# Kernel tuning notes

Measured on AMD Instinct MI355X. Metric: run time of the kernel, lower is better.

Reference implementation:

```python
import jax, jax.numpy as jnp
import numpy as np

B, S, D = 2, 2048, 1024
H, E = 16, 64


def setup_inputs() -> dict:
    key = jax.random.key(0)
    k1, k2, k3, k4 = jax.random.split(key, 4)
    x = jax.random.normal(k1, (B, S, D), dtype=jnp.float32)
    # per-head Q/K/V projection weights, stacked over the head axis
    scale = 1.0 / np.sqrt(D)
    Wq = jax.random.normal(k2, (H, D, E), dtype=jnp.float32) * scale
    Wk = jax.random.normal(k3, (H, D, E), dtype=jnp.float32) * scale
    Wv = jax.random.normal(k4, (H, D, E), dtype=jnp.float32) * scale
    return {"x": x, "Wq": Wq, "Wk": Wk, "Wv": Wv}


def reference(x, Wq, Wk, Wv):
    # Grouped-over-heads equivalent of the per-head torch loop.
    q = jnp.einsum("bsd,hde->bhse", x, Wq)  # [B,H,S,E]
    k = jnp.einsum("bsd,hde->bhse", x, Wk)
    v = jnp.einsum("bsd,hde->bhse", x, Wv)

    scores = jnp.einsum("bhse,bhte->bhst", q, k)  # [B,H,S,S]
    scores = scores / jnp.sqrt(jnp.asarray(E, dtype=scores.dtype))
    causal = jnp.tril(jnp.ones((S, S), dtype=bool))  # True on/below diagonal
    scores = jnp.where(causal, scores, jnp.finfo(scores.dtype).min)
    attn = jax.nn.softmax(scores, axis=-1)  # dropout p=0.0 -> identity

    out = jnp.einsum("bhst,bhte->bhse", attn, v)  # [B,H,S,E]
    # concat over heads on the last dim, matching torch.concat(..., dim=-1)
    return out.transpose(0, 2, 1, 3).reshape(B, S, H * E)
```

## Files before the change

### kernel.cpp

```cpp
#include <hip/hip_runtime.h>
#include <stdint.h>

#define S_LEN 2048
#define D_DIM 1024
#define NB 2
#define NH 16
#define NE 64
#define N_COLS (3 * NH * NE)
#define K_DIM D_DIM

typedef unsigned short u16;
typedef unsigned int u32;
typedef u16 u16x8 __attribute__((ext_vector_type(8)));
typedef __bf16 bf16x8 __attribute__((ext_vector_type(8)));
typedef __bf16 bf16x4 __attribute__((ext_vector_type(4)));
typedef float f32x4 __attribute__((ext_vector_type(4)));

__device__ __forceinline__ u16 f2b(float f) {
  u32 u = __builtin_bit_cast(u32, f);
  return (u16)((u + 0x7FFFu + ((u >> 16) & 1u)) >> 16);
}

__device__ __forceinline__ void gload_lds16(const void* g, void* l) {
  __builtin_amdgcn_global_load_lds(
      (const __attribute__((address_space(1))) u32*)g,
      (__attribute__((address_space(3))) u32*)l, 16, 0, 0);
}

__global__ __launch_bounds__(256) void k_prep(const float* __restrict__ x,
                                              const float* __restrict__ Wq,
                                              const float* __restrict__ Wk,
                                              const float* __restrict__ Wv,
                                              u16* __restrict__ xb,
                                              u16* __restrict__ Wt) {
  __shared__ u16 tile[64][65];
  int bid = blockIdx.x;
  int t = threadIdx.x;
  if (bid < 2048) {
    size_t i = (size_t)bid * 256 + t;
    const float4* xf = (const float4*)x;
    float4 a = xf[2 * i], c = xf[2 * i + 1];
    u16x8 o;
    o[0] = f2b(a.x); o[1] = f2b(a.y); o[2] = f2b(a.z); o[3] = f2b(a.w);
    o[4] = f2b(c.x); o[5] = f2b(c.y); o[6] = f2b(c.z); o[7] = f2b(c.w);
    *(u16x8*)(xb + 8 * i) = o;
  } else {
    int wbid = bid - 2048;
    int kb = wbid & 15;
    int h = (wbid >> 4) & 15;
    int proj = wbid >> 8;
    const float* W = (proj == 0) ? Wq : ((proj == 1) ? Wk : Wv);
    int k0 = kb * 64;
    int e = t & 63, kr = t >> 6;
    const float* src = W + ((size_t)h * D_DIM + k0 + kr * 16) * NE + e;
#pragma unroll
    for (int j = 0; j < 16; ++j) tile[kr * 16 + j][e] = f2b(src[(size_t)j * NE]);
    __syncthreads();
    int e2 = t >> 2, kc = (t & 3) * 16;
    u16x8 o0, o1;
#pragma unroll
    for (int j = 0; j < 8; ++j) { o0[j] = tile[kc + j][e2]; o1[j] = tile[kc + 8 + j][e2]; }
    size_t n = (size_t)proj * 1024 + h * 64 + e2;
    u16* dst = Wt + n * K_DIM + k0 + kc;
    *(u16x8*)dst = o0;
    *(u16x8*)(dst + 8) = o1;
  }
}

__global__ __launch_bounds__(256) void k_gemm(const u16* __restrict__ A,
                                              const u16* __restrict__ Bt,
                                              u16* __restrict__ C) {
  __shared__ __align__(16) u16 As[128 * 64];
  __shared__ __align__(16) u16 Bs[128 * 64];
  int t = threadIdx.x;
  int lane = t & 63, w = t >> 6;
  int wr = (w >> 1) * 64, wc = (w & 1) * 64;
  int bid = blockIdx.x;
  int xcd = bid & 7, r0 = bid >> 3;
  int m0 = (r0 / 3) * 128;
  int n0 = (xcd * 3 + (r0 % 3)) * 128;
  float qscale = ((n0 + wc) < 1024) ? 0.18033688f : 1.0f;
  f32x4 acc[4][4];
#pragma unroll
  for (int m = 0; m < 4; m++)
#pragma unroll
    for (int n = 0; n < 4; n++)
#pragma unroll
      for (int j = 0; j < 4; j++) acc[m][n][j] = 0.f;

  for (int k0 = 0; k0 < K_DIM; k0 += 64) {
#pragma unroll
    for (int i = 0; i < 4; ++i) {
      int ci = i * 256 + t;
      int row = ci >> 3, c = ci & 7;
      int cs = c ^ (row & 7);
      gload_lds16(A + (size_t)(m0 + row) * K_DIM + k0 + cs * 8,
                  (char*)As + (size_t)(i * 256 + w * 64) * 16);
      gload_lds16(Bt + (size_t)(n0 + row) * K_DIM + k0 + cs * 8,
                  (char*)Bs + (size_t)(i * 256 + w * 64) * 16);
    }
    __syncthreads();
#pragma unroll
    for (int ks = 0; ks < 2; ++ks) {
      int kc = ks * 4 + (lane >> 4);
      bf16x8 af[4], bfr[4];
#pragma unroll
      for (int m = 0; m < 4; m++) {
        int r = wr + m * 16 + (lane & 15);
        af[m] = *(const bf16x8*)&As[r * 64 + ((kc ^ (r & 7)) * 8)];
      }
#pragma unroll
      for (int n = 0; n < 4; n++) {
        int r = wc + n * 16 + (lane & 15);
        bfr[n] = *(const bf16x8*)&Bs[r * 64 + ((kc ^ (r & 7)) * 8)];
      }
#pragma unroll
      for (int m = 0; m < 4; m++)
#pragma unroll
        for (int n = 0; n < 4; n++)
          acc[m][n] = __builtin_amdgcn_mfma_f32_16x16x32_bf16(af[m], bfr[n], acc[m][n], 0, 0, 0);
    }
    __syncthreads();
  }
#pragma unroll
  for (int m = 0; m < 4; m++) {
#pragma unroll
    for (int r = 0; r < 4; r++) {
      int row = m0 + wr + m * 16 + (lane >> 4) * 4 + r;
#pragma unroll
      for (int n = 0; n < 4; n++) {
        int col = n0 + wc + n * 16 + (lane & 15);
        C[(size_t)row * N_COLS + col] = f2b(acc[m][n][r] * qscale);
      }
    }
  }
}

__device__ __forceinline__ void stage_k(const u16* kb_, u16* kdst, int kv0, int t, int w) {
#pragma unroll
  for (int i = 0; i < 2; ++i) {
    int ci = i * 256 + t;
    int row = ci >> 3, c = ci & 7;
    int cs = c ^ (row & 7);
    gload_lds16(kb_ + (size_t)(kv0 + row) * N_COLS + cs * 8,
                (char*)kdst + (size_t)(i * 256 + w * 64) * 16);
  }
}

__device__ __forceinline__ void vwrite(u16* vt, u16x8 va, u16x8 vb2, int vp, int vec) {
#pragma unroll
  for (int j = 0; j < 8; ++j) {
    int e = vec * 8 + j;
    int slot = (vp >> 2) ^ (e & 7) ^ (e >> 3);
    *(u32*)((char*)vt + e * 128 + slot * 16 + (vp & 3) * 4) =
        (u32)va[j] | ((u32)vb2[j] << 16);
  }
}

__global__ __launch_bounds__(256) void k_attn(const u16* __restrict__ qkv,
                                              float* __restrict__ out) {
  __shared__ __align__(16) u16 Ks[2][64 * 64];
  __shared__ __align__(16) u16 Vt[2][64 * 64];
  int t = threadIdx.x;
  int lane = t & 63, w = t >> 6;
  int hi = lane >> 4, l15 = lane & 15;
  int bid = blockIdx.x;
  int x = bid & 7, g = bid >> 3;
  int bh = x * 4 + (g & 3);
  int qt = 31 - (g >> 2);
  int b = bh >> 4, h = bh & 15;
  const u16* qb_ = qkv + (size_t)b * S_LEN * N_COLS + h * NE;
  const u16* kb_ = qb_ + 1024;
  const u16* vb_ = qb_ + 2048;
  int vp = t >> 3, vec = t & 7;

  int q0 = qt * 64;
  int nt = qt + 1;
  int wqb = q0 + w * 16;

  bf16x8 qf[2];
#pragma unroll
  for (int ks = 0; ks < 2; ks++)
    qf[ks] = *(const bf16x8*)(qb_ + (size_t)(wqb + l15) * N_COLS + ks * 32 + hi * 8);

  f32x4 o[4];
#pragma unroll
  for (int i = 0; i < 4; i++)
#pragma unroll
    for (int j = 0; j < 4; j++) o[i][j] = 0.f;
  float lsum = 0.f;
  int myq = wqb + l15;

  stage_k(kb_, Ks[0], 0, t, w);
  {
    const u16* vs = vb_ + (size_t)(2 * vp) * N_COLS + vec * 8;
    u16x8 va = *(const u16x8*)vs;
    u16x8 vb2 = *(const u16x8*)(vs + N_COLS);
    vwrite(Vt[0], va, vb2, vp, vec);
  }
  __syncthreads();

  int cur = 0;
  for (int ti = 0; ti < nt; ++ti) {
    int kv0 = ti * 64;
    bool pf = (ti + 1 < nt);
    u16x8 va, vb2;
    if (pf) {
      const u16* vs = vb_ + (size_t)(kv0 + 64 + 2 * vp) * N_COLS + vec * 8;
      va = *(const u16x8*)vs;
      vb2 = *(const u16x8*)(vs + N_COLS);
      stage_k(kb_, Ks[cur ^ 1], kv0 + 64, t, w);
    }

    f32x4 s[4];
#pragma unroll
    for (int f = 0; f < 4; f++)
#pragma unroll
      for (int j = 0; j < 4; j++) s[f][j] = 0.f;
    __builtin_amdgcn_s_setprio(1);
#pragma unroll
    for (int ks = 0; ks < 2; ks++) {
      int kc = ks * 4 + hi;
#pragma unroll
      for (int f = 0; f < 4; f++) {
        int r = f * 16 + l15;
        bf16x8 kf = *(const bf16x8*)&Ks[cur][r * 64 + ((kc ^ (r & 7)) * 8)];
        s[f] = __builtin_amdgcn_mfma_f32_16x16x32_bf16(kf, qf[ks], s[f], 0, 0, 0);
      }
    }
    __builtin_amdgcn_s_setprio(0);

    bool diag = (ti == nt - 1);
#pragma unroll
    for (int f = 0; f < 4; f++) {
#pragma unroll
      for (int r = 0; r < 4; r++) {
        float p = __builtin_amdgcn_exp2f(s[f][r]);
        if (diag) {
          int kv = kv0 + f * 16 + 4 * hi + r;
          p = (kv <= myq) ? p : 0.f;
        }
        s[f][r] = p;
        lsum += p;
      }
    }

    if (pf) vwrite(Vt[cur ^ 1], va, vb2, vp, vec);

    __builtin_amdgcn_s_setprio(1);
#pragma unroll
    for (int ks = 0; ks < 2; ks++) {
      bf16x8 pa;
#pragma unroll
      for (int j = 0; j < 4; j++) {
        pa[j] = (__bf16)s[2 * ks][j];
        pa[4 + j] = (__bf16)s[2 * ks + 1][j];
      }
      int kvo1 = 32 * ks + 4 * hi;
      int kvo2 = kvo1 + 16;
#pragma unroll
      for (int ef = 0; ef < 4; ef++) {
        int e = ef * 16 + l15;
        int sw = (e & 7) ^ (e >> 3);
        int a1 = e * 128 + (((kvo1 >> 3) ^ sw) * 16) + (kvo1 & 7) * 2;
        int a2 = e * 128 + (((kvo2 >> 3) ^ sw) * 16) + (kvo2 & 7) * 2;
        bf16x4 vlo = *(const bf16x4*)((const char*)Vt[cur] + a1);
        bf16x4 vhi = *(const bf16x4*)((const char*)Vt[cur] + a2);
        bf16x8 vbf;
#pragma unroll
        for (int j = 0; j < 4; j++) { vbf[j] = vlo[j]; vbf[4 + j] = vhi[j]; }
        o[ef] = __builtin_amdgcn_mfma_f32_16x16x32_bf16(pa, vbf, o[ef], 0, 0, 0);
      }
    }
    __builtin_amdgcn_s_setprio(0);
    __syncthreads();
    cur ^= 1;
  }

  lsum += __shfl_xor(lsum, 16);
  lsum += __shfl_xor(lsum, 32);
#pragma unroll
  for (int r = 0; r < 4; r++) {
    float l = __shfl(lsum, 4 * hi + r);
    float inv = 1.0f / l;
    int q = wqb + 4 * hi + r;
#pragma unroll
    for (int ef = 0; ef < 4; ef++) {
      int col = h * NE + ef * 16 + l15;
      out[((size_t)b * S_LEN + q) * (NH * NE) + col] = o[ef][r] * inv;
    }
  }
}

extern "C" void kernel_launch(void* const* d_in, const int* in_sizes, int n_in,
                              void* d_out, int out_size, void* d_ws, size_t ws_size,
                              hipStream_t stream) {
  const float* x = (const float*)d_in[0];
  const float* Wq = (const float*)d_in[1];
  const float* Wk = (const float*)d_in[2];
  const float* Wv = (const float*)d_in[3];
  float* out = (float*)d_out;

  char* ws = (char*)d_ws;
  u16* xb = (u16*)ws;
  u16* Wt = (u16*)(ws + (8u << 20));
  u16* qkv = (u16*)(ws + (14u << 20));

  k_prep<<<dim3(2816), dim3(256), 0, stream>>>(x, Wq, Wk, Wv, xb, Wt);
  k_gemm<<<dim3(768), dim3(256), 0, stream>>>(xb, Wt, qkv);
  k_attn<<<dim3(1024), dim3(256), 0, stream>>>(qkv, out);
}
```

Measured before the change: 93.92 us.

## Split KV range of long causal query tiles across two blocks with a fixup kernel

Measured after the change: 100.2 us. +6.7%, slower.

```diff
diff --git a/kernel.cpp b/kernel.cpp
--- a/kernel.cpp
+++ b/kernel.cpp
@@ -158,16 +158,27 @@
 }
 
 __global__ __launch_bounds__(256) void k_attn(const u16* __restrict__ qkv,
-                                              float* __restrict__ out) {
+                                              float* __restrict__ out,
+                                              float* __restrict__ O0,
+                                              float* __restrict__ l0,
+                                              float* __restrict__ l1) {
   __shared__ __align__(16) u16 Ks[2][64 * 64];
   __shared__ __align__(16) u16 Vt[2][64 * 64];
   int t = threadIdx.x;
   int lane = t & 63, w = t >> 6;
   int hi = lane >> 4, l15 = lane & 15;
   int bid = blockIdx.x;
-  int x = bid & 7, g = bid >> 3;
-  int bh = x * 4 + (g & 3);
-  int qt = 31 - (g >> 2);
+  int x = bid & 7, r_ = bid >> 3;
+  int bh = x * 4 + (r_ & 3);
+  int u = r_ >> 2;
+  int qt, c;
+  if (u < 32) { qt = 31 - (u >> 1); c = u & 1; }
+  else        { qt = 47 - u;        c = 0;     }
+  int nt = qt + 1;
+  int halfn = (nt + 1) >> 1;
+  bool split = (u < 32);
+  int lo = (split && c) ? halfn : 0;
+  int te = split ? (c ? nt : halfn) : nt;
   int b = bh >> 4, h = bh & 15;
   const u16* qb_ = qkv + (size_t)b * S_LEN * N_COLS + h * NE;
   const u16* kb_ = qb_ + 1024;
@@ -175,7 +186,6 @@
   int vp = t >> 3, vec = t & 7;
 
   int q0 = qt * 64;
-  int nt = qt + 1;
   int wqb = q0 + w * 16;
 
   bf16x8 qf[2];
@@ -191,9 +201,9 @@
   float lsum = 0.f;
   int myq = wqb + l15;
 
-  stage_k(kb_, Ks[0], 0, t, w);
+  stage_k(kb_, Ks[0], lo * 64, t, w);
   {
-    const u16* vs = vb_ + (size_t)(2 * vp) * N_COLS + vec * 8;
+    const u16* vs = vb_ + (size_t)(lo * 64 + 2 * vp) * N_COLS + vec * 8;
     u16x8 va = *(const u16x8*)vs;
     u16x8 vb2 = *(const u16x8*)(vs + N_COLS);
     vwrite(Vt[0], va, vb2, vp, vec);
@@ -201,9 +211,9 @@
   __syncthreads();
 
   int cur = 0;
-  for (int ti = 0; ti < nt; ++ti) {
+  for (int ti = lo; ti < te; ++ti) {
     int kv0 = ti * 64;
-    bool pf = (ti + 1 < nt);
+    bool pf = (ti + 1 < te);
     u16x8 va, vb2;
     if (pf) {
       const u16* vs = vb_ + (size_t)(kv0 + 64 + 2 * vp) * N_COLS + vec * 8;
@@ -279,17 +289,66 @@
 
   lsum += __shfl_xor(lsum, 16);
   lsum += __shfl_xor(lsum, 32);
-#pragma unroll
-  for (int r = 0; r < 4; r++) {
-    float l = __shfl(lsum, 4 * hi + r);
-    float inv = 1.0f / l;
-    int q = wqb + 4 * hi + r;
-#pragma unroll
-    for (int ef = 0; ef < 4; ef++) {
-      int col = h * NE + ef * 16 + l15;
-      out[((size_t)b * S_LEN + q) * (NH * NE) + col] = o[ef][r] * inv;
-    }
-  }
+
+  if (!split) {
+#pragma unroll
+    for (int r = 0; r < 4; r++) {
+      float l = __shfl(lsum, 4 * hi + r);
+      float inv = 1.0f / l;
+      int q = wqb + 4 * hi + r;
+#pragma unroll
+      for (int ef = 0; ef < 4; ef++) {
+        int col = h * NE + ef * 16 + l15;
+        out[((size_t)b * S_LEN + q) * (NH * NE) + col] = o[ef][r] * inv;
+      }
+    }
+  } else {
+    int sp = bh * 16 + (qt - 16);
+    if (c == 0) {
+#pragma unroll
+      for (int r = 0; r < 4; r++) {
+        int row = w * 16 + 4 * hi + r;
+#pragma unroll
+        for (int ef = 0; ef < 4; ef++)
+          O0[(size_t)sp * 4096 + row * 64 + ef * 16 + l15] = o[ef][r];
+      }
+      if (lane < 16) l0[sp * 64 + w * 16 + l15] = lsum;
+    } else {
+#pragma unroll
+      for (int r = 0; r < 4; r++) {
+        int q = wqb + 4 * hi + r;
+#pragma unroll
+        for (int ef = 0; ef < 4; ef++) {
+          int col = h * NE + ef * 16 + l15;
+          out[((size_t)b * S_LEN + q) * (NH * NE) + col] = o[ef][r];
+        }
+      }
+      if (lane < 16) l1[sp * 64 + w * 16 + l15] = lsum;
+    }
+  }
+}
+
+__global__ __launch_bounds__(256) void k_fix(float* __restrict__ out,
+                                             const float* __restrict__ O0,
+                                             const float* __restrict__ l0,
+                                             const float* __restrict__ l1) {
+  int f = (blockIdx.x * 256 + threadIdx.x) * 4;
+  int sp = f >> 12;
+  int row = (f >> 6) & 63;
+  int e0 = f & 63;
+  int bh = sp >> 4, qt = 16 + (sp & 15);
+  int b = bh >> 4, h = bh & 15;
+  int q = qt * 64 + row;
+  float inv = 1.0f / (l0[sp * 64 + row] + l1[sp * 64 + row]);
+  float4 p0 = *(const float4*)&O0[(size_t)sp * 4096 + row * 64 + e0];
+  size_t oi = ((size_t)b * S_LEN + q) * (NH * NE) + h * NE + e0;
+  float4 cu = *(float4*)&out[oi];
+  float4 res;
+  res.x = (cu.x + p0.x) * inv;
+  res.y = (cu.y + p0.y) * inv;
+  res.z = (cu.z + p0.z) * inv;
+  res.w = (cu.w + p0.w) * inv;
+  *(float4*)&out[oi] = res;
 }
 
 extern "C" void kernel_launch(void* const* d_in, const int* in_sizes, int n_in,
@@ -305,8 +364,12 @@
   u16* xb = (u16*)ws;
   u16* Wt = (u16*)(ws + (8u << 20));
   u16* qkv = (u16*)(ws + (14u << 20));
+  float* O0 = (float*)ws;
+  float* l0 = (float*)(ws + (8u << 20));
+  float* l1 = (float*)(ws + (8u << 20) + (128u << 10));
 
   k_prep<<<dim3(2816), dim3(256), 0, stream>>>(x, Wq, Wk, Wv, xb, Wt);
   k_gemm<<<dim3(768), dim3(256), 0, stream>>>(xb, Wt, qkv);
-  k_attn<<<dim3(1024), dim3(256), 0, stream>>>(qkv, out);
-}
+  k_attn<<<dim3(1536), dim3(256), 0, stream>>>(qkv, out, O0, l0, l1);
+  k_fix<<<dim3(2048), dim3(256), 0, stream>>>(out, O0, l0, l1);
+}
```

## Process two 64-row query tiles per attention block to reuse K/V tiles

Applied to the files above, without the earlier changes.

Result: slower. 132.1 us (+40.7%).

```diff
diff --git a/kernel.cpp b/kernel.cpp
--- a/kernel.cpp
+++ b/kernel.cpp
@@ -13,7 +13,6 @@
 typedef unsigned int u32;
 typedef u16 u16x8 __attribute__((ext_vector_type(8)));
 typedef __bf16 bf16x8 __attribute__((ext_vector_type(8)));
-typedef __bf16 bf16x4 __attribute__((ext_vector_type(4)));
 typedef float f32x4 __attribute__((ext_vector_type(4)));
 
 __device__ __forceinline__ u16 f2b(float f) {
@@ -147,12 +146,14 @@
   }
 }
 
-__device__ __forceinline__ void vwrite(u16* vt, u16x8 va, u16x8 vb2, int vp, int vec) {
+__device__ __forceinline__ void vwrite(u16* vt, u16x8 va, u16x8 vb2, int kvA, int vec) {
+  int pi_hi = ((kvA >> 5) << 2) | ((kvA & 15) >> 2);
+  int pi_lo = (kvA & 3) * 4;
 #pragma unroll
   for (int j = 0; j < 8; ++j) {
     int e = vec * 8 + j;
-    int slot = (vp >> 2) ^ (e & 7) ^ (e >> 3);
-    *(u32*)((char*)vt + e * 128 + slot * 16 + (vp & 3) * 4) =
+    int sw = (e & 7) ^ (e >> 3);
+    *(u32*)((char*)vt + e * 128 + ((pi_hi ^ sw) * 16) + pi_lo) =
         (u32)va[j] | ((u32)vb2[j] << 16);
   }
 }
@@ -167,36 +168,39 @@
   int bid = blockIdx.x;
   int x = bid & 7, g = bid >> 3;
   int bh = x * 4 + (g & 3);
-  int qt = 31 - (g >> 2);
+  int qb = 15 - (g >> 2);
   int b = bh >> 4, h = bh & 15;
   const u16* qb_ = qkv + (size_t)b * S_LEN * N_COLS + h * NE;
   const u16* kb_ = qb_ + 1024;
   const u16* vb_ = qb_ + 2048;
-  int vp = t >> 3, vec = t & 7;
-
-  int q0 = qt * 64;
-  int nt = qt + 1;
-  int wqb = q0 + w * 16;
-
-  bf16x8 qf[2];
-#pragma unroll
-  for (int ks = 0; ks < 2; ks++)
-    qf[ks] = *(const bf16x8*)(qb_ + (size_t)(wqb + l15) * N_COLS + ks * 32 + hi * 8);
-
-  f32x4 o[4];
+  int w2 = t >> 3, vec = t & 7;
+  int kvA0 = (w2 & 15) | ((w2 & 16) << 1);
+
+  int q0 = qb * 128;
+  int nt = 2 * qb + 2;
+  int wqA = q0 + w * 16;
+  int myqA = wqA + l15, myqB = myqA + 64;
+
+  bf16x8 qfA[2], qfB[2];
+#pragma unroll
+  for (int ks = 0; ks < 2; ks++) {
+    qfA[ks] = *(const bf16x8*)(qb_ + (size_t)(wqA + l15) * N_COLS + ks * 32 + hi * 8);
+    qfB[ks] = *(const bf16x8*)(qb_ + (size_t)(wqA + 64 + l15) * N_COLS + ks * 32 + hi * 8);
+  }
+
+  f32x4 oA[4], oB[4];
 #pragma unroll
   for (int i = 0; i < 4; i++)
 #pragma unroll
-    for (int j = 0; j < 4; j++) o[i][j] = 0.f;
-  float lsum = 0.f;
-  int myq = wqb + l15;
+    for (int j = 0; j < 4; j++) { oA[i][j] = 0.f; oB[i][j] = 0.f; }
+  float lsA = 0.f, lsB = 0.f;
 
   stage_k(kb_, Ks[0], 0, t, w);
   {
-    const u16* vs = vb_ + (size_t)(2 * vp) * N_COLS + vec * 8;
+    const u16* vs = vb_ + (size_t)kvA0 * N_COLS + vec * 8;
     u16x8 va = *(const u16x8*)vs;
-    u16x8 vb2 = *(const u16x8*)(vs + N_COLS);
-    vwrite(Vt[0], va, vb2, vp, vec);
+    u16x8 vb2 = *(const u16x8*)(vs + 16 * N_COLS);
+    vwrite(Vt[0], va, vb2, kvA0, vec);
   }
   __syncthreads();
 
@@ -206,17 +210,20 @@
     bool pf = (ti + 1 < nt);
     u16x8 va, vb2;
     if (pf) {
-      const u16* vs = vb_ + (size_t)(kv0 + 64 + 2 * vp) * N_COLS + vec * 8;
+      const u16* vs = vb_ + (size_t)(kv0 + 64 + kvA0) * N_COLS + vec * 8;
       va = *(const u16x8*)vs;
-      vb2 = *(const u16x8*)(vs + N_COLS);
+      vb2 = *(const u16x8*)(vs + 16 * N_COLS);
       stage_k(kb_, Ks[cur ^ 1], kv0 + 64, t, w);
     }
-
-    f32x4 s[4];
+    bool doA = (ti != nt - 1);
+    bool maskA = (ti == nt - 2);
+    bool maskB = (ti == nt - 1);
+
+    f32x4 sA[4], sB[4];
 #pragma unroll
     for (int f = 0; f < 4; f++)
 #pragma unroll
-      for (int j = 0; j < 4; j++) s[f][j] = 0.f;
+      for (int j = 0; j < 4; j++) { sA[f][j] = 0.f; sB[f][j] = 0.f; }
     __builtin_amdgcn_s_setprio(1);
 #pragma unroll
     for (int ks = 0; ks < 2; ks++) {
@@ -225,51 +232,60 @@
       for (int f = 0; f < 4; f++) {
         int r = f * 16 + l15;
         bf16x8 kf = *(const bf16x8*)&Ks[cur][r * 64 + ((kc ^ (r & 7)) * 8)];
-        s[f] = __builtin_amdgcn_mfma_f32_16x16x32_bf16(kf, qf[ks], s[f], 0, 0, 0);
+        sB[f] = __builtin_amdgcn_mfma_f32_16x16x32_bf16(kf, qfB[ks], sB[f], 0, 0, 0);
+        if (doA)
+          sA[f] = __builtin_amdgcn_mfma_f32_16x16x32_bf16(kf, qfA[ks], sA[f], 0, 0, 0);
       }
     }
     __builtin_amdgcn_s_setprio(0);
 
-    bool diag = (ti == nt - 1);
-#pragma unroll
-    for (int f = 0; f < 4; f++) {
+    if (doA) {
+#pragma unroll
+      for (int f = 0; f < 4; f++)
+#pragma unroll
+        for (int r = 0; r < 4; r++) {
+          float p = __builtin_amdgcn_exp2f(sA[f][r]);
+          if (maskA) {
+            int kv = kv0 + f * 16 + 4 * hi + r;
+            p = (kv <= myqA) ? p : 0.f;
+          }
+          sA[f][r] = p;
+          lsA += p;
+        }
+    }
+#pragma unroll
+    for (int f = 0; f < 4; f++)
 #pragma unroll
       for (int r = 0; r < 4; r++) {
-        float p = __builtin_amdgcn_exp2f(s[f][r]);
-        if (diag) {
+        float p = __builtin_amdgcn_exp2f(sB[f][r]);
+        if (maskB) {
           int kv = kv0 + f * 16 + 4 * hi + r;
-          p = (kv <= myq) ? p : 0.f;
+          p = (kv <= myqB) ? p : 0.f;
         }
-        s[f][r] = p;
-        lsum += p;
-      }
-    }
-
-    if (pf) vwrite(Vt[cur ^ 1], va, vb2, vp, vec);
+        sB[f][r] = p;
+        lsB += p;
+      }
+
+    if (pf) vwrite(Vt[cur ^ 1], va, vb2, kvA0, vec);
 
     __builtin_amdgcn_s_setprio(1);
 #pragma unroll
     for (int ks = 0; ks < 2; ks++) {
-      bf16x8 pa;
-#pragma unroll
-      for (int j = 0; j < 4; j++) {
-        pa[j] = (__bf16)s[2 * ks][j];
-        pa[4 + j] = (__bf16)s[2 * ks + 1][j];
-      }
-      int kvo1 = 32 * ks + 4 * hi;
-      int kvo2 = kvo1 + 16;
+      bf16x8 paA, paB;
+#pragma unroll
+      for (int d = 0; d < 8; d++) {
+        paA[d] = (__bf16)sA[2 * ks + (d & 1)][d >> 1];
+        paB[d] = (__bf16)sB[2 * ks + (d & 1)][d >> 1];
+      }
 #pragma unroll
       for (int ef = 0; ef < 4; ef++) {
         int e = ef * 16 + l15;
         int sw = (e & 7) ^ (e >> 3);
-        int a1 = e * 128 + (((kvo1 >> 3) ^ sw) * 16) + (kvo1 & 7) * 2;
-        int a2 = e * 128 + (((kvo2 >> 3) ^ sw) * 16) + (kvo2 & 7) * 2;
-        bf16x4 vlo = *(const bf16x4*)((const char*)Vt[cur] + a1);
-        bf16x4 vhi = *(const bf16x4*)((const char*)Vt[cur] + a2);
-        bf16x8 vbf;
-#pragma unroll
-        for (int j = 0; j < 4; j++) { vbf[j] = vlo[j]; vbf[4 + j] = vhi[j]; }
-        o[ef] = __builtin_amdgcn_mfma_f32_16x16x32_bf16(pa, vbf, o[ef], 0, 0, 0);
+        bf16x8 vbf = *(const bf16x8*)((const char*)Vt[cur] + e * 128 +
+                                      (((4 * ks + hi) ^ sw) * 16));
+        oB[ef] = __builtin_amdgcn_mfma_f32_16x16x32_bf16(paB, vbf, oB[ef], 0, 0, 0);
+        if (doA)
+          oA[ef] = __builtin_amdgcn_mfma_f32_16x16x32_bf16(paA, vbf, oA[ef], 0, 0, 0);
       }
     }
     __builtin_amdgcn_s_setprio(0);
@@ -277,17 +293,22 @@
     cur ^= 1;
   }
 
-  lsum += __shfl_xor(lsum, 16);
-  lsum += __shfl_xor(lsum, 32);
+  lsA += __shfl_xor(lsA, 16);
+  lsA += __shfl_xor(lsA, 32);
+  lsB += __shfl_xor(lsB, 16);
+  lsB += __shfl_xor(lsB, 32);
 #pragma unroll
   for (int r = 0; r < 4; r++) {
-    float l = __shfl(lsum, 4 * hi + r);
-    float inv = 1.0f / l;
-    int q = wqb + 4 * hi + r;
+    float la = __shfl(lsA, 4 * hi + r);
+    float lb = __shfl(lsB, 4 * hi + r);
+    float invA = 1.0f / la, invB = 1.0f / lb;
+    int qA = wqA + 4 * hi + r;
 #pragma unroll
     for (int ef = 0; ef < 4; ef++) {
       int col = h * NE + ef * 16 + l15;
-      out[((size_t)b * S_LEN + q) * (NH * NE) + col] = o[ef][r] * inv;
+      size_t base = (size_t)b * S_LEN;
+      out[(base + qA) * (NH * NE) + col] = oA[ef][r] * invA;
+      out[(base + qA + 64) * (NH * NE) + col] = oB[ef][r] * invB;
     }
   }
 }
@@ -308,5 +329,5 @@
 
   k_prep<<<dim3(2816), dim3(256), 0, stream>>>(x, Wq, Wk, Wv, xb, Wt);
   k_gemm<<<dim3(768), dim3(256), 0, stream>>>(xb, Wt, qkv);
-  k_attn<<<dim3(1024), dim3(256), 0, stream>>>(qkv, out);
-}
+  k_attn<<<dim3(512), dim3(256), 0, stream>>>(qkv, out);
+}
```

## Write V transposed and kv-permuted from GEMM epilogue; stage V via async LDS loads

Applied to the files above, without the earlier changes.

New measurement: 86.29 us. 1.09x faster.

```diff
diff --git a/kernel.cpp b/kernel.cpp
--- a/kernel.cpp
+++ b/kernel.cpp
@@ -7,13 +7,14 @@
 #define NH 16
 #define NE 64
 #define N_COLS (3 * NH * NE)
+#define QK_COLS 2048
 #define K_DIM D_DIM
 
 typedef unsigned short u16;
 typedef unsigned int u32;
+typedef unsigned long long u64;
 typedef u16 u16x8 __attribute__((ext_vector_type(8)));
 typedef __bf16 bf16x8 __attribute__((ext_vector_type(8)));
-typedef __bf16 bf16x4 __attribute__((ext_vector_type(4)));
 typedef float f32x4 __attribute__((ext_vector_type(4)));
 
 __device__ __forceinline__ u16 f2b(float f) {
@@ -69,16 +70,19 @@
 
 __global__ __launch_bounds__(256) void k_gemm(const u16* __restrict__ A,
                                               const u16* __restrict__ Bt,
-                                              u16* __restrict__ C) {
+                                              u16* __restrict__ Cqk,
+                                              u16* __restrict__ VT) {
   __shared__ __align__(16) u16 As[128 * 64];
   __shared__ __align__(16) u16 Bs[128 * 64];
   int t = threadIdx.x;
   int lane = t & 63, w = t >> 6;
+  int hi = lane >> 4, l15 = lane & 15;
   int wr = (w >> 1) * 64, wc = (w & 1) * 64;
   int bid = blockIdx.x;
   int xcd = bid & 7, r0 = bid >> 3;
   int m0 = (r0 / 3) * 128;
   int n0 = (xcd * 3 + (r0 % 3)) * 128;
+  bool isV = (n0 >= 2048);
   float qscale = ((n0 + wc) < 1024) ? 0.18033688f : 1.0f;
   f32x4 acc[4][4];
 #pragma unroll
@@ -102,16 +106,16 @@
     __syncthreads();
 #pragma unroll
     for (int ks = 0; ks < 2; ++ks) {
-      int kc = ks * 4 + (lane >> 4);
+      int kc = ks * 4 + hi;
       bf16x8 af[4], bfr[4];
 #pragma unroll
       for (int m = 0; m < 4; m++) {
-        int r = wr + m * 16 + (lane & 15);
+        int r = wr + m * 16 + l15;
         af[m] = *(const bf16x8*)&As[r * 64 + ((kc ^ (r & 7)) * 8)];
       }
 #pragma unroll
       for (int n = 0; n < 4; n++) {
-        int r = wc + n * 16 + (lane & 15);
+        int r = wc + n * 16 + l15;
         bfr[n] = *(const bf16x8*)&Bs[r * 64 + ((kc ^ (r & 7)) * 8)];
       }
 #pragma unroll
@@ -122,15 +126,33 @@
     }
     __syncthreads();
   }
-#pragma unroll
-  for (int m = 0; m < 4; m++) {
-#pragma unroll
-    for (int r = 0; r < 4; r++) {
-      int row = m0 + wr + m * 16 + (lane >> 4) * 4 + r;
+
+  if (!isV) {
+#pragma unroll
+    for (int m = 0; m < 4; m++) {
+#pragma unroll
+      for (int r = 0; r < 4; r++) {
+        int row = m0 + wr + m * 16 + hi * 4 + r;
+#pragma unroll
+        for (int n = 0; n < 4; n++) {
+          int col = n0 + wc + n * 16 + l15;
+          Cqk[(size_t)row * QK_COLS + col] = f2b(acc[m][n][r] * qscale);
+        }
+      }
+    }
+  } else {
+#pragma unroll
+    for (int m = 0; m < 4; m++) {
+      int row_s = m0 + wr + m * 16 + hi * 4;
+      int bb = row_s >> 11, s = row_s & 2047;
+      int pos = (s & ~63) | (s & 32) | ((s & 12) << 1) | ((s & 16) >> 2) | (s & 3);
 #pragma unroll
       for (int n = 0; n < 4; n++) {
-        int col = n0 + wc + n * 16 + (lane & 15);
-        C[(size_t)row * N_COLS + col] = f2b(acc[m][n][r] * qscale);
+        int col = n0 + wc + n * 16 + l15 - 2048;
+        int hh = col >> 6, e = col & 63;
+        u64 pk = (u64)f2b(acc[m][n][0]) | ((u64)f2b(acc[m][n][1]) << 16) |
+                 ((u64)f2b(acc[m][n][2]) << 32) | ((u64)f2b(acc[m][n][3]) << 48);
+        *(u64*)(VT + ((size_t)((bb * 16 + hh) * 64 + e)) * S_LEN + pos) = pk;
       }
     }
   }
@@ -142,25 +164,27 @@
     int ci = i * 256 + t;
     int row = ci >> 3, c = ci & 7;
     int cs = c ^ (row & 7);
-    gload_lds16(kb_ + (size_t)(kv0 + row) * N_COLS + cs * 8,
+    gload_lds16(kb_ + (size_t)(kv0 + row) * QK_COLS + cs * 8,
                 (char*)kdst + (size_t)(i * 256 + w * 64) * 16);
   }
 }
 
-__device__ __forceinline__ void vwrite(u16* vt, u16x8 va, u16x8 vb2, int vp, int vec) {
-#pragma unroll
-  for (int j = 0; j < 8; ++j) {
-    int e = vec * 8 + j;
-    int slot = (vp >> 2) ^ (e & 7) ^ (e >> 3);
-    *(u32*)((char*)vt + e * 128 + slot * 16 + (vp & 3) * 4) =
-        (u32)va[j] | ((u32)vb2[j] << 16);
-  }
-}
-
-__global__ __launch_bounds__(256) void k_attn(const u16* __restrict__ qkv,
+__device__ __forceinline__ void stage_v(const u16* vtb_, u16* vdst, int kv0, int t, int w) {
+#pragma unroll
+  for (int i = 0; i < 2; ++i) {
+    int ci = i * 256 + t;
+    int row = ci >> 3, c = ci & 7;
+    int cs = c ^ (row & 7);
+    gload_lds16(vtb_ + (size_t)row * S_LEN + kv0 + cs * 8,
+                (char*)vdst + (size_t)(i * 256 + w * 64) * 16);
+  }
+}
+
+__global__ __launch_bounds__(256) void k_attn(const u16* __restrict__ qk,
+                                              const u16* __restrict__ VT,
                                               float* __restrict__ out) {
   __shared__ __align__(16) u16 Ks[2][64 * 64];
-  __shared__ __align__(16) u16 Vt[2][64 * 64];
+  __shared__ __align__(16) u16 Vs[2][64 * 64];
   int t = threadIdx.x;
   int lane = t & 63, w = t >> 6;
   int hi = lane >> 4, l15 = lane & 15;
@@ -169,10 +193,9 @@
   int bh = x * 4 + (g & 3);
   int qt = 31 - (g >> 2);
   int b = bh >> 4, h = bh & 15;
-  const u16* qb_ = qkv + (size_t)b * S_LEN * N_COLS + h * NE;
+  const u16* qb_ = qk + (size_t)b * S_LEN * QK_COLS + h * NE;
   const u16* kb_ = qb_ + 1024;
-  const u16* vb_ = qb_ + 2048;
-  int vp = t >> 3, vec = t & 7;
+  const u16* vtb_ = VT + (size_t)bh * 64 * S_LEN;
 
   int q0 = qt * 64;
   int nt = qt + 1;
@@ -181,7 +204,7 @@
   bf16x8 qf[2];
 #pragma unroll
   for (int ks = 0; ks < 2; ks++)
-    qf[ks] = *(const bf16x8*)(qb_ + (size_t)(wqb + l15) * N_COLS + ks * 32 + hi * 8);
+    qf[ks] = *(const bf16x8*)(qb_ + (size_t)(wqb + l15) * QK_COLS + ks * 32 + hi * 8);
 
   f32x4 o[4];
 #pragma unroll
@@ -192,24 +215,16 @@
   int myq = wqb + l15;
 
   stage_k(kb_, Ks[0], 0, t, w);
-  {
-    const u16* vs = vb_ + (size_t)(2 * vp) * N_COLS + vec * 8;
-    u16x8 va = *(const u16x8*)vs;
-    u16x8 vb2 = *(const u16x8*)(vs + N_COLS);
-    vwrite(Vt[0], va, vb2, vp, vec);
-  }
+  stage_v(vtb_, Vs[0], 0, t, w);
   __syncthreads();
 
   int cur = 0;
   for (int ti = 0; ti < nt; ++ti) {
     int kv0 = ti * 64;
     bool pf = (ti + 1 < nt);
-    u16x8 va, vb2;
     if (pf) {
-      const u16* vs = vb_ + (size_t)(kv0 + 64 + 2 * vp) * N_COLS + vec * 8;
-      va = *(const u16x8*)vs;
-      vb2 = *(const u16x8*)(vs + N_COLS);
       stage_k(kb_, Ks[cur ^ 1], kv0 + 64, t, w);
+      stage_v(vtb_, Vs[cur ^ 1], kv0 + 64, t, w);
     }
 
     f32x4 s[4];
@@ -245,8 +260,6 @@
       }
     }
 
-    if (pf) vwrite(Vt[cur ^ 1], va, vb2, vp, vec);
-
     __builtin_amdgcn_s_setprio(1);
 #pragma unroll
     for (int ks = 0; ks < 2; ks++) {
@@ -256,19 +269,10 @@
         pa[j] = (__bf16)s[2 * ks][j];
         pa[4 + j] = (__bf16)s[2 * ks + 1][j];
       }
-      int kvo1 = 32 * ks + 4 * hi;
-      int kvo2 = kvo1 + 16;
 #pragma unroll
       for (int ef = 0; ef < 4; ef++) {
         int e = ef * 16 + l15;
-        int sw = (e & 7) ^ (e >> 3);
-        int a1 = e * 128 + (((kvo1 >> 3) ^ sw) * 16) + (kvo1 & 7) * 2;
-        int a2 = e * 128 + (((kvo2 >> 3) ^ sw) * 16) + (kvo2 & 7) * 2;
-        bf16x4 vlo = *(const bf16x4*)((const char*)Vt[cur] + a1);
-        bf16x4 vhi = *(const bf16x4*)((const char*)Vt[cur] + a2);
-        bf16x8 vbf;
-#pragma unroll
-        for (int j = 0; j < 4; j++) { vbf[j] = vlo[j]; vbf[4 + j] = vhi[j]; }
+        bf16x8 vbf = *(const bf16x8*)&Vs[cur][e * 64 + (((4 * ks + hi) ^ (e & 7)) * 8)];
         o[ef] = __builtin_amdgcn_mfma_f32_16x16x32_bf16(pa, vbf, o[ef], 0, 0, 0);
       }
     }
@@ -304,9 +308,10 @@
   char* ws = (char*)d_ws;
   u16* xb = (u16*)ws;
   u16* Wt = (u16*)(ws + (8u << 20));
-  u16* qkv = (u16*)(ws + (14u << 20));
+  u16* qk = (u16*)(ws + (14u << 20));
+  u16* VT = (u16*)(ws + (30u << 20));
 
   k_prep<<<dim3(2816), dim3(256), 0, stream>>>(x, Wq, Wk, Wv, xb, Wt);
-  k_gemm<<<dim3(768), dim3(256), 0, stream>>>(xb, Wt, qkv);
-  k_attn<<<dim3(1024), dim3(256), 0, stream>>>(qkv, out);
-}
+  k_gemm<<<dim3(768), dim3(256), 0, stream>>>(xb, Wt, qk, VT);
+  k_attn<<<dim3(1024), dim3(256), 0, stream>>>(qk, VT, out);
+}
```
